# Optimization experiments

Hardware: AMD Instinct MI355X
Metric: run time of the kernel (lower is better)

Reference implementation:

```python
import jax, jax.numpy as jnp
import numpy as np

IN_DIM = 256
OUT_DIM = 256
B, N, E = 8, 1024, 262144
K_RATIO = 0.5
BN_EPS = 1e-5


def _xavier(key, shape):
    fan_in, fan_out = shape[1], shape[0]
    lim = float(np.sqrt(6.0 / (fan_in + fan_out)))
    return jax.random.uniform(key, shape, jnp.float32, -lim, lim)


def setup_inputs() -> dict:
    key = jax.random.key(0)
    ks = jax.random.split(key, 10)
    x = jax.random.normal(ks[0], (B, N, IN_DIM), jnp.float32)
    edges = jax.random.randint(ks[1], (2, E), 0, B * N, jnp.int64 if jax.config.jax_enable_x64 else jnp.int32)
    return {
        "x": x,
        "edges": edges,
        "att_proj_w": _xavier(ks[2], (OUT_DIM, IN_DIM)),
        "att_proj_b": jnp.zeros((OUT_DIM,), jnp.float32),
        "att_map_w": _xavier(ks[3], (1, OUT_DIM)).reshape(OUT_DIM),
        "pwa_w": _xavier(ks[4], (OUT_DIM, IN_DIM)),
        "pwa_b": jnp.zeros((OUT_DIM,), jnp.float32),
        "pwo_w": _xavier(ks[5], (OUT_DIM, IN_DIM)),
        "pwo_b": jnp.zeros((OUT_DIM,), jnp.float32),
        "bn_gamma": jnp.ones((OUT_DIM,), jnp.float32),
        "bn_beta": jnp.zeros((OUT_DIM,), jnp.float32),
        "y_w": _xavier(ks[6], (1, OUT_DIM)).reshape(OUT_DIM),
        "y_b": jnp.zeros((), jnp.float32),
    }


def reference(x, edges, att_proj_w, att_proj_b, att_map_w, pwa_w, pwa_b,
              pwo_w, pwo_b, bn_gamma, bn_beta, y_w, y_b):
    b, n, d = x.shape
    num_nodes = b * n
    xf = x.reshape(num_nodes, d)
    src, dst = edges[0], edges[1]  # x_j = source, x_i = destination

    # --- GAT message: alpha = att_map(tanh(att_proj(x_i * x_j))) ---
    x_j = xf[src]                                # [E, d]
    x_i = xf[dst]                                # [E, d]
    h = jnp.tanh((x_i * x_j) @ att_proj_w.T + att_proj_b)  # [E, out]
    alpha = h @ att_map_w                        # [E]

    # --- segment softmax over destination nodes ---
    amax = jax.ops.segment_max(alpha, dst, num_segments=num_nodes)
    a = jnp.exp(alpha - amax[dst])
    denom = jax.ops.segment_sum(a, dst, num_segments=num_nodes)
    w = a / (denom[dst] + 1e-16)

    # --- scatter-sum aggregate of alpha * x_j ---
    agg = jax.ops.segment_sum(w[:, None] * x_j, dst, num_segments=num_nodes)  # [num_nodes, d]

    out = agg @ pwa_w.T + pwa_b + xf @ pwo_w.T + pwo_b  # [num_nodes, out]

    # --- BatchNorm1d (training-mode batch stats, biased var) + SELU ---
    mean = out.mean(axis=0)
    var = out.var(axis=0)
    out = (out - mean) * jax.lax.rsqrt(var + BN_EPS) * bn_gamma + bn_beta
    out = jax.nn.selu(out)

    out = out.reshape(b, n, -1)  # [B, N, out]

    # --- GraphPool: top-k by sigmoid score, gate by score ---
    y = jax.nn.sigmoid(out @ y_w + y_b)  # [B, N]
    k = max(int(n * K_RATIO), 1)
    vals, ids = jax.lax.top_k(y, k)      # [B, k]
    x_top = jnp.take_along_axis(out, ids[..., None], axis=1)  # [B, k, out]
    return x_top * vals[..., None]
```

## Files before the change

kernel.cpp:

```cpp
#include <hip/hip_runtime.h>
#include <math.h>

#define NODES 8192
#define NEDGE 262144
#define DIM 256

typedef float f32x16 __attribute__((ext_vector_type(16)));
typedef _Float16 f16x8 __attribute__((ext_vector_type(8)));
typedef unsigned short u16;
typedef u16 u16x8 __attribute__((ext_vector_type(8)));
typedef u16 u16x4 __attribute__((ext_vector_type(4)));

__device__ __forceinline__ float fast_tanh(float x) {
    float t = __expf(2.f * x);
    return 1.f - 2.f * __builtin_amdgcn_rcpf(t + 1.f);
}

__device__ __forceinline__ u16 h_bits(_Float16 h) {
    u16 r; __builtin_memcpy(&r, &h, 2); return r;
}

__global__ void k_deg(const int* __restrict__ dst, int* __restrict__ deg) {
    int e = blockIdx.x * blockDim.x + threadIdx.x;
    if (e < NEDGE) atomicAdd(&deg[dst[e]], 1);
}

__global__ void k_scan(const int* __restrict__ deg, int* __restrict__ rowptr,
                       int* __restrict__ cursor) {
    __shared__ int part[256];
    int t = threadIdx.x;
    int base = t * 32;
    int local[32];
    int s = 0;
    for (int i = 0; i < 32; ++i) { local[i] = s; s += deg[base + i]; }
    part[t] = s;
    __syncthreads();
    for (int off = 1; off < 256; off <<= 1) {
        int v = (t >= off) ? part[t - off] : 0;
        __syncthreads();
        part[t] += v;
        __syncthreads();
    }
    int excl = (t == 0) ? 0 : part[t - 1];
    for (int i = 0; i < 32; ++i) {
        int v = excl + local[i];
        rowptr[base + i] = v;
        cursor[base + i] = v;
    }
    if (t == 255) rowptr[NODES] = part[255];
}

__global__ void k_fill(const int* __restrict__ src, const int* __restrict__ dst,
                       int* __restrict__ cursor, int2* __restrict__ sdg) {
    int e = blockIdx.x * blockDim.x + threadIdx.x;
    if (e < NEDGE) {
        int pos = atomicAdd(&cursor[dst[e]], 1);
        sdg[pos] = make_int2(src[e], dst[e]);
    }
}

__global__ void k_wfrag(const float* __restrict__ W, u16* __restrict__ wf) {
    int t = blockIdx.x * blockDim.x + threadIdx.x;
    if (t >= 16 * 4 * 2 * 64) return;
    int lane = t & 63;
    int mt = (t >> 6) & 1;
    int w = (t >> 7) & 3;
    int gks = t >> 9;
    int row = w * 64 + mt * 32 + (lane & 31);
    int k0 = gks * 16 + (lane >> 5) * 8;
    const float* p = W + (size_t)row * DIM + k0;
    u16x8 v1, v2;
#pragma unroll
    for (int j = 0; j < 8; ++j) {
        float f = p[j];
        _Float16 h1 = (_Float16)f;
        _Float16 h2 = (_Float16)((f - (float)h1) * 2048.f);
        v1[j] = h_bits(h1);
        v2[j] = h_bits(h2);
    }
    size_t base = ((size_t)(gks * 4 + w) * 4 + mt * 2) * 512 + lane * 8;
    *(u16x8*)(wf + base)       = v1;
    *(u16x8*)(wf + base + 512) = v2;
}

__global__ void k_wfrag2(const float* __restrict__ Wa, const float* __restrict__ Wo,
                         u16* __restrict__ wf2) {
    int t = blockIdx.x * blockDim.x + threadIdx.x;
    if (t >= 32 * 4 * 2 * 64) return;
    int lane = t & 63;
    int mt = (t >> 6) & 1;
    int w = (t >> 7) & 3;
    int gks = t >> 9;
    const float* W = (gks < 16) ? Wa : Wo;
    int row = w * 64 + mt * 32 + (lane & 31);
    int k0 = (gks & 15) * 16 + (lane >> 5) * 8;
    const float* p = W + (size_t)row * DIM + k0;
    u16x8 v1, v2;
#pragma unroll
    for (int j = 0; j < 8; ++j) {
        float f = p[j];
        _Float16 h1 = (_Float16)f;
        _Float16 h2 = (_Float16)((f - (float)h1) * 2048.f);
        v1[j] = h_bits(h1);
        v2[j] = h_bits(h2);
    }
    size_t base = ((size_t)(gks * 4 + w) * 4 + mt * 2) * 512 + lane * 8;
    *(u16x8*)(wf2 + base)       = v1;
    *(u16x8*)(wf2 + base + 512) = v2;
}

__global__ __launch_bounds__(256, 2) void k_alpha_v12(
    const float* __restrict__ x, const int2* __restrict__ sdg,
    const u16* __restrict__ wf, const float* __restrict__ bias,
    const float* __restrict__ amap, float* __restrict__ alpha_pos)
{
    __shared__ u16 p_lds[2][64][256];
    const int tid = threadIdx.x;
    const int w = tid >> 6;
    const int lane = tid & 63;
    const int l31 = lane & 31;
    const int g2 = lane >> 5;
    const int bid = blockIdx.x;
    const int wg = (bid & 7) * 512 + (bid >> 3);
    const int e0 = wg * 64;
    const int ebase = e0 + w * 16;
    const unsigned swz = ((unsigned)(l31 & 7)) << 4;

    f32x16 accM[2][2], accC[2][2];
#pragma unroll
    for (int mt = 0; mt < 2; ++mt)
#pragma unroll
        for (int nt = 0; nt < 2; ++nt) { accM[mt][nt] = (f32x16)0.f; accC[mt][nt] = (f32x16)0.f; }

    f16x8 afA[2][2], afB[2][2], afC[2][2];

#define PREFA(DST, GKS) { \
    const u16* pb_ = wf + ((size_t)((GKS) * 4 + w) * 4) * 512 + lane * 8; \
    _Pragma("unroll") for (int mt_ = 0; mt_ < 2; ++mt_) \
    _Pragma("unroll") for (int pl_ = 0; pl_ < 2; ++pl_) \
        DST[mt_][pl_] = *(const f16x8*)(const void*)(pb_ + (mt_ * 2 + pl_) * 512); }

#define KS(GKS, USE, PF) { \
    if ((GKS) + 2 < 16) { PREFA(PF, (GKS) + 2) } \
    f16x8 bfr[2][2]; \
    _Pragma("unroll") for (int nt_ = 0; nt_ < 2; ++nt_) { \
        const int en_ = nt_ * 32 + l31; \
        const unsigned off_ = ((unsigned)((GKS) * 32 + g2 * 16)) ^ swz; \
        _Pragma("unroll") for (int pl_ = 0; pl_ < 2; ++pl_) \
            bfr[nt_][pl_] = *(const f16x8*)(const void*)((const char*)&p_lds[pl_][en_][0] + off_); \
    } \
    _Pragma("unroll") for (int mt_ = 0; mt_ < 2; ++mt_) \
    _Pragma("unroll") for (int nt_ = 0; nt_ < 2; ++nt_) { \
        accM[mt_][nt_] = __builtin_amdgcn_mfma_f32_32x32x16_f16(USE[mt_][0], bfr[nt_][0], accM[mt_][nt_], 0, 0, 0); \
        accC[mt_][nt_] = __builtin_amdgcn_mfma_f32_32x32x16_f16(USE[mt_][0], bfr[nt_][1], accC[mt_][nt_], 0, 0, 0); \
        accC[mt_][nt_] = __builtin_amdgcn_mfma_f32_32x32x16_f16(USE[mt_][1], bfr[nt_][0], accC[mt_][nt_], 0, 0, 0); } }

    PREFA(afA, 0)
    PREFA(afB, 1)

#pragma unroll
    for (int i = 0; i < 16; ++i) {
        int2 sd = sdg[ebase + i];
        float4 a = *(const float4*)(x + (size_t)sd.x * DIM + lane * 4);
        float4 b = *(const float4*)(x + (size_t)sd.y * DIM + lane * 4);
        float pv[4] = {a.x * b.x, a.y * b.y, a.z * b.z, a.w * b.w};
        u16x4 v1, v2;
#pragma unroll
        for (int j = 0; j < 4; ++j) {
            float f = pv[j];
            _Float16 h1 = (_Float16)f;
            _Float16 h2 = (_Float16)((f - (float)h1) * 2048.f);
            v1[j] = h_bits(h1);
            v2[j] = h_bits(h2);
        }
        const int le = w * 16 + i;
        const unsigned off = ((unsigned)(lane * 8)) ^ (((unsigned)(le & 7)) << 4);
        *(u16x4*)((char*)&p_lds[0][le][0] + off) = v1;
        *(u16x4*)((char*)&p_lds[1][le][0] + off) = v2;
    }
    __syncthreads();

    KS(0,  afA, afC) KS(1,  afB, afA) KS(2,  afC, afB)
    KS(3,  afA, afC) KS(4,  afB, afA) KS(5,  afC, afB)
    KS(6,  afA, afC) KS(7,  afB, afA) KS(8,  afC, afB)
    KS(9,  afA, afC) KS(10, afB, afA) KS(11, afC, afB)
    KS(12, afA, afC) KS(13, afB, afA) KS(14, afC, afB)
    KS(15, afA, afC)
#undef KS
#undef PREFA

    float part[2] = {0.f, 0.f};
#pragma unroll
    for (int mt = 0; mt < 2; ++mt)
#pragma unroll
        for (int r = 0; r < 16; ++r) {
            int o = 64 * w + 32 * mt + (r & 3) + 8 * (r >> 2) + 4 * g2;
            float bo = bias[o], ao = amap[o];
#pragma unroll
            for (int nt = 0; nt < 2; ++nt) {
                float h = accM[mt][nt][r] + accC[mt][nt][r] * 4.8828125e-4f;
                part[nt] += ao * fast_tanh(h + bo);
            }
        }
    __syncthreads();
    float* red = (float*)(void*)p_lds;
#pragma unroll
    for (int nt = 0; nt < 2; ++nt) {
        float p = part[nt];
        p += __shfl_xor(p, 32);
        if (lane < 32) red[w * 64 + nt * 32 + lane] = p;
    }
    __syncthreads();
    if (tid < 64) alpha_pos[e0 + tid] = red[tid] + red[64 + tid] + red[128 + tid] + red[192 + tid];
}

__global__ void k_aggregate(
    const float* __restrict__ x, const float* __restrict__ alpha_pos,
    const int* __restrict__ rowptr, const int2* __restrict__ sdg,
    float* __restrict__ agg)
{
    int gw = (blockIdx.x * blockDim.x + threadIdx.x) >> 6;
    int lane = threadIdx.x & 63;
    if (gw >= NODES) return;
    int start = rowptr[gw], end = rowptr[gw + 1];
    int deg = end - start;
    float m = -INFINITY;
    for (int i = lane; i < deg; i += 64) m = fmaxf(m, alpha_pos[start + i]);
#pragma unroll
    for (int off = 32; off > 0; off >>= 1) m = fmaxf(m, __shfl_xor(m, off));
    float ssum = 0.f;
    for (int i = lane; i < deg; i += 64) ssum += expf(alpha_pos[start + i] - m);
#pragma unroll
    for (int off = 32; off > 0; off >>= 1) ssum += __shfl_xor(ssum, off);
    float a0 = 0.f, a1 = 0.f, a2 = 0.f, a3 = 0.f;
    int i = 0;
    for (; i + 4 <= deg; i += 4) {
        float w0 = expf(alpha_pos[start + i]     - m);
        float w1 = expf(alpha_pos[start + i + 1] - m);
        float w2 = expf(alpha_pos[start + i + 2] - m);
        float w3 = expf(alpha_pos[start + i + 3] - m);
        int r0 = sdg[start + i].x;
        int r1 = sdg[start + i + 1].x;
        int r2 = sdg[start + i + 2].x;
        int r3 = sdg[start + i + 3].x;
        float4 v0 = *(const float4*)(x + (size_t)r0 * DIM + lane * 4);
        float4 v1 = *(const float4*)(x + (size_t)r1 * DIM + lane * 4);
        float4 v2 = *(const float4*)(x + (size_t)r2 * DIM + lane * 4);
        float4 v3 = *(const float4*)(x + (size_t)r3 * DIM + lane * 4);
        a0 += w0 * v0.x + w1 * v1.x + w2 * v2.x + w3 * v3.x;
        a1 += w0 * v0.y + w1 * v1.y + w2 * v2.y + w3 * v3.y;
        a2 += w0 * v0.z + w1 * v1.z + w2 * v2.z + w3 * v3.z;
        a3 += w0 * v0.w + w1 * v1.w + w2 * v2.w + w3 * v3.w;
    }
    for (; i < deg; ++i) {
        float wgt = expf(alpha_pos[start + i] - m);
        int r = sdg[start + i].x;
        const float4 v = *(const float4*)(x + (size_t)r * DIM + lane * 4);
        a0 += wgt * v.x; a1 += wgt * v.y; a2 += wgt * v.z; a3 += wgt * v.w;
    }
    float inv = 1.f / (ssum + 1e-16f);
    float4 r; r.x = a0 * inv; r.y = a1 * inv; r.z = a2 * inv; r.w = a3 * inv;
    *(float4*)(agg + (size_t)gw * DIM + lane * 4) = r;
}

__global__ __launch_bounds__(256, 2) void k_out_mfma(
    const float* __restrict__ agg, const float* __restrict__ x,
    const u16* __restrict__ wf2, const float* __restrict__ ba,
    const float* __restrict__ bo, float* __restrict__ outb)
{
    __shared__ u16 p_lds[2][64][256];
    const int tid = threadIdx.x;
    const int w = tid >> 6;
    const int lane = tid & 63;
    const int l31 = lane & 31;
    const int g2 = lane >> 5;
    const int n0 = blockIdx.x * 64;
    const unsigned swz = ((unsigned)(l31 & 7)) << 4;

    f32x16 accM[2][2], accC[2][2];
#pragma unroll
    for (int mt = 0; mt < 2; ++mt)
#pragma unroll
        for (int nt = 0; nt < 2; ++nt) { accM[mt][nt] = (f32x16)0.f; accC[mt][nt] = (f32x16)0.f; }

    f16x8 afA[2][2], afB[2][2];

#define PREFA2(DST, GKS) { \
    const u16* pb_ = wf2 + ((size_t)((GKS) * 4 + w) * 4) * 512 + lane * 8; \
    _Pragma("unroll") for (int mt_ = 0; mt_ < 2; ++mt_) \
    _Pragma("unroll") for (int pl_ = 0; pl_ < 2; ++pl_) \
        DST[mt_][pl_] = *(const f16x8*)(const void*)(pb_ + (mt_ * 2 + pl_) * 512); }

#define OSTAGE(SRC) { \
    _Pragma("unroll") for (int i_ = 0; i_ < 16; ++i_) { \
        const int ln_ = w * 16 + i_; \
        float4 v_ = *(const float4*)((SRC) + (size_t)(n0 + ln_) * DIM + lane * 4); \
        float pv_[4] = {v_.x, v_.y, v_.z, v_.w}; \
        u16x4 v1_, v2_; \
        _Pragma("unroll") for (int j_ = 0; j_ < 4; ++j_) { \
            float f_ = pv_[j_]; \
            _Float16 h1_ = (_Float16)f_; \
            _Float16 h2_ = (_Float16)((f_ - (float)h1_) * 2048.f); \
            v1_[j_] = h_bits(h1_); v2_[j_] = h_bits(h2_); } \
        const unsigned off_ = ((unsigned)(lane * 8)) ^ (((unsigned)(ln_ & 7)) << 4); \
        *(u16x4*)((char*)&p_lds[0][ln_][0] + off_) = v1_; \
        *(u16x4*)((char*)&p_lds[1][ln_][0] + off_) = v2_; } }

#define OKSTEP(GKS) { \
    if ((GKS) + 1 < 32) { \
        if ((GKS) & 1) { PREFA2(afA, (GKS) + 1) } else { PREFA2(afB, (GKS) + 1) } \
    } \
    f16x8 bfr[2][2]; \
    _Pragma("unroll") for (int nt_ = 0; nt_ < 2; ++nt_) { \
        const int en_ = nt_ * 32 + l31; \
        const unsigned off_ = ((unsigned)(((GKS) & 15) * 32 + g2 * 16)) ^ swz; \
        _Pragma("unroll") for (int pl_ = 0; pl_ < 2; ++pl_) \
            bfr[nt_][pl_] = *(const f16x8*)(const void*)((const char*)&p_lds[pl_][en_][0] + off_); \
    } \
    _Pragma("unroll") for (int mt_ = 0; mt_ < 2; ++mt_) \
    _Pragma("unroll") for (int nt_ = 0; nt_ < 2; ++nt_) { \
        f16x8 a1_ = ((GKS) & 1) ? afB[mt_][0] : afA[mt_][0]; \
        f16x8 a2_ = ((GKS) & 1) ? afB[mt_][1] : afA[mt_][1]; \
        accM[mt_][nt_] = __builtin_amdgcn_mfma_f32_32x32x16_f16(a1_, bfr[nt_][0], accM[mt_][nt_], 0, 0, 0); \
        accC[mt_][nt_] = __builtin_amdgcn_mfma_f32_32x32x16_f16(a1_, bfr[nt_][1], accC[mt_][nt_], 0, 0, 0); \
        accC[mt_][nt_] = __builtin_amdgcn_mfma_f32_32x32x16_f16(a2_, bfr[nt_][0], accC[mt_][nt_], 0, 0, 0); } }

    PREFA2(afA, 0)
    OSTAGE(agg)
    __syncthreads();
    OKSTEP(0)  OKSTEP(1)  OKSTEP(2)  OKSTEP(3)
    OKSTEP(4)  OKSTEP(5)  OKSTEP(6)  OKSTEP(7)
    OKSTEP(8)  OKSTEP(9)  OKSTEP(10) OKSTEP(11)
    OKSTEP(12) OKSTEP(13) OKSTEP(14) OKSTEP(15)
    __syncthreads();
    OSTAGE(x)
    __syncthreads();
    OKSTEP(16) OKSTEP(17) OKSTEP(18) OKSTEP(19)
    OKSTEP(20) OKSTEP(21) OKSTEP(22) OKSTEP(23)
    OKSTEP(24) OKSTEP(25) OKSTEP(26) OKSTEP(27)
    OKSTEP(28) OKSTEP(29) OKSTEP(30) OKSTEP(31)
#undef OSTAGE
#undef OKSTEP
#undef PREFA2

    __syncthreads();
    float* Cs = (float*)(void*)p_lds;
#pragma unroll
    for (int mt = 0; mt < 2; ++mt)
#pragma unroll
        for (int r = 0; r < 16; ++r) {
            int o = 64 * w + 32 * mt + (r & 3) + 8 * (r >> 2) + 4 * g2;
            float bs = ba[o] + bo[o];
#pragma unroll
            for (int nt = 0; nt < 2; ++nt) {
                int col = nt * 32 + l31;
                float hv = accM[mt][nt][r] + accC[mt][nt][r] * 4.8828125e-4f + bs;
                unsigned ob = ((unsigned)(col * 1024 + o * 4)) ^ (((unsigned)(col & 31)) << 4);
                *(float*)((char*)Cs + ob) = hv;
            }
        }
    __syncthreads();
#pragma unroll
    for (int i = 0; i < 16; ++i) {
        int ln = w * 16 + i;
        unsigned rb = ((unsigned)(ln * 1024 + lane * 16)) ^ (((unsigned)(ln & 31)) << 4);
        float4 val = *(const float4*)((const char*)Cs + rb);
        *(float4*)(outb + (size_t)(n0 + ln) * DIM + lane * 4) = val;
    }
}

__global__ void k_colstat(const float* __restrict__ outb, double* __restrict__ psum,
                          double* __restrict__ psq) {
    int g = blockIdx.x, t = threadIdx.x;
    double s = 0.0, q = 0.0;
    const float* p = outb + (size_t)g * 256 * DIM + t;
    for (int r = 0; r < 256; ++r) { double v = (double)p[(size_t)r * DIM]; s += v; q += v * v; }
    psum[g * DIM + t] = s;
    psq[g * DIM + t] = q;
}

__global__ void k_bnparam(const double* __restrict__ psum, const double* __restrict__ psq,
                          const float* __restrict__ gamma, const float* __restrict__ beta,
                          float* __restrict__ scale, float* __restrict__ shift) {
    int t = threadIdx.x;
    double s = 0.0, q = 0.0;
    for (int g = 0; g < 32; ++g) { s += psum[g * DIM + t]; q += psq[g * DIM + t]; }
    double mean = s / (double)NODES;
    double var = q / (double)NODES - mean * mean;
    float sc = (float)((double)gamma[t] / sqrt(var + 1e-5));
    scale[t] = sc;
    shift[t] = (float)((double)beta[t] - mean * (double)sc);
}

__global__ void k_bnselu(float* __restrict__ outb, const float* __restrict__ scale,
                         const float* __restrict__ shift, const float* __restrict__ yw,
                         const float* __restrict__ yb, float* __restrict__ y) {
    int gw = (blockIdx.x * blockDim.x + threadIdx.x) >> 6;
    int lane = threadIdx.x & 63;
    if (gw >= NODES) return;
    float4 v  = *(const float4*)(outb + (size_t)gw * DIM + lane * 4);
    float4 sc = *(const float4*)(scale + lane * 4);
    float4 sh = *(const float4*)(shift + lane * 4);
    const float SL = 1.0507009873554805f, SA = 1.6732632423543772f;
    float4 o;
    o.x = v.x * sc.x + sh.x;
    o.y = v.y * sc.y + sh.y;
    o.z = v.z * sc.z + sh.z;
    o.w = v.w * sc.w + sh.w;
    o.x = (o.x > 0.f) ? SL * o.x : SL * SA * expm1f(o.x);
    o.y = (o.y > 0.f) ? SL * o.y : SL * SA * expm1f(o.y);
    o.z = (o.z > 0.f) ? SL * o.z : SL * SA * expm1f(o.z);
    o.w = (o.w > 0.f) ? SL * o.w : SL * SA * expm1f(o.w);
    *(float4*)(outb + (size_t)gw * DIM + lane * 4) = o;
    float4 w = *(const float4*)(yw + lane * 4);
    float z = o.x * w.x + o.y * w.y + o.z * w.z + o.w * w.w;
#pragma unroll
    for (int off = 32; off > 0; off >>= 1) z += __shfl_xor(z, off);
    if (lane == 0) y[gw] = 1.f / (1.f + expf(-(z + yb[0])));
}

__global__ void k_topk(const float* __restrict__ y, float* __restrict__ svals,
                       int* __restrict__ sidx) {
    __shared__ float v[1024];
    __shared__ int  id[1024];
    int b = blockIdx.x, t = threadIdx.x;
    v[t] = y[b * 1024 + t];           id[t] = t;
    v[t + 512] = y[b * 1024 + t + 512]; id[t + 512] = t + 512;
    __syncthreads();
    for (int k = 2; k <= 1024; k <<= 1) {
        for (int j = k >> 1; j > 0; j >>= 1) {
            for (int i = t; i < 1024; i += 512) {
                int l = i ^ j;
                if (l > i) {
                    float vi = v[i], vl = v[l];
                    int ii = id[i], il = id[l];
                    bool precede = (vi > vl) || (vi == vl && ii < il);
                    bool dirDesc = ((i & k) == 0);
                    bool sw = dirDesc ? !precede : precede;
                    if (sw) { v[i] = vl; v[l] = vi; id[i] = il; id[l] = ii; }
                }
            }
            __syncthreads();
        }
    }
    if (t < 512) { svals[b * 512 + t] = v[t]; sidx[b * 512 + t] = id[t]; }
}

__global__ void k_gather(const float* __restrict__ outb, const float* __restrict__ svals,
                         const int* __restrict__ sidx, float* __restrict__ dout) {
    int gw = (blockIdx.x * blockDim.x + threadIdx.x) >> 6;
    int lane = threadIdx.x & 63;
    int b = gw >> 9, r = gw & 511;
    float val = svals[b * 512 + r];
    int idn = sidx[b * 512 + r];
    float4 vv = *(const float4*)(outb + (size_t)(b * 1024 + idn) * DIM + lane * 4);
    vv.x *= val; vv.y *= val; vv.z *= val; vv.w *= val;
    *(float4*)(dout + (size_t)(b * 512 + r) * DIM + lane * 4) = vv;
}

extern "C" void kernel_launch(void* const* d_in, const int* in_sizes, int n_in,
                              void* d_out, int out_size, void* d_ws, size_t ws_size,
                              hipStream_t stream) {
    const float* x     = (const float*)d_in[0];
    const int* edges   = (const int*)d_in[1];
    const float* att_w = (const float*)d_in[2];
    const float* att_b = (const float*)d_in[3];
    const float* amap  = (const float*)d_in[4];
    const float* pwa_w = (const float*)d_in[5];
    const float* pwa_b = (const float*)d_in[6];
    const float* pwo_w = (const float*)d_in[7];
    const float* pwo_b = (const float*)d_in[8];
    const float* gamma = (const float*)d_in[9];
    const float* beta  = (const float*)d_in[10];
    const float* yw    = (const float*)d_in[11];
    const float* yb    = (const float*)d_in[12];
    float* out = (float*)d_out;
    const int* src = edges;
    const int* dst = edges + NEDGE;

    char* ws = (char*)d_ws;
    size_t off = 0;
    auto alloc = [&](size_t b) { void* p = ws + off; off = (off + b + 255) & ~(size_t)255; return p; };
    float* alpha  = (float*)alloc((size_t)NEDGE * 4);
    int2*  sdg    = (int2*)alloc((size_t)NEDGE * 8);
    float* agg    = (float*)alloc((size_t)NODES * DIM * 4);
    float* outb   = (float*)alloc((size_t)NODES * DIM * 4);
    int*   deg    = (int*)alloc(NODES * 4);
    int*   rowptr = (int*)alloc((NODES + 1) * 4);
    int*   cursor = (int*)alloc(NODES * 4);
    double* psum  = (double*)alloc(32 * DIM * 8);
    double* psq   = (double*)alloc(32 * DIM * 8);
    float* scale  = (float*)alloc(DIM * 4);
    float* shift  = (float*)alloc(DIM * 4);
    float* yv     = (float*)alloc(NODES * 4);
    float* svals  = (float*)alloc(8 * 512 * 4);
    int*   sidx   = (int*)alloc(8 * 512 * 4);
    u16*   wf     = (u16*)alloc((size_t)16 * 4 * 4 * 512 * 2);
    u16*   wf2    = (u16*)alloc((size_t)32 * 4 * 4 * 512 * 2);

    hipMemsetAsync(deg, 0, NODES * 4, stream);
    k_wfrag<<<32, 256, 0, stream>>>(att_w, wf);
    k_wfrag2<<<64, 256, 0, stream>>>(pwa_w, pwo_w, wf2);
    k_deg<<<NEDGE / 256, 256, 0, stream>>>(dst, deg);
    k_scan<<<1, 256, 0, stream>>>(deg, rowptr, cursor);
    k_fill<<<NEDGE / 256, 256, 0, stream>>>(src, dst, cursor, sdg);
    k_alpha_v12<<<NEDGE / 64, 256, 0, stream>>>(x, sdg, wf, att_b, amap, alpha);
    k_aggregate<<<NODES / 4, 256, 0, stream>>>(x, alpha, rowptr, sdg, agg);
    k_out_mfma<<<NODES / 64, 256, 0, stream>>>(agg, x, wf2, pwa_b, pwo_b, outb);
    k_colstat<<<32, 256, 0, stream>>>(outb, psum, psq);
    k_bnparam<<<1, 256, 0, stream>>>(psum, psq, gamma, beta, scale, shift);
    k_bnselu<<<NODES / 4, 256, 0, stream>>>(outb, scale, shift, yw, yb, yv);
    k_topk<<<8, 512, 0, stream>>>(yv, svals, sidx);
    k_gather<<<(8 * 512) / 4, 256, 0, stream>>>(outb, svals, sidx, out);
}
```

Measured before the change: 266.5 us.

## Warp-specialize alpha kernel into producer gather waves and MFMA consumer waves

Splits the alpha kernel's 512-thread block into four producer waves and four consumer waves. The producers gather x rows, form the elementwise products, split them into fp16 hi/lo parts and write them into double-buffered LDS half-tiles. The consumers run the MFMA tanh projection, so the gather of the next tile overlaps compute on the current one. Each block now handles 256 edges across four tiles, and each consumer wave writes its own partial alpha sum to global memory. A new small kernel adds the four partials, which costs extra global traffic and a launch, plus a block-wide barrier at every stage.

```diff
diff --git a/kernel.cpp b/kernel.cpp
--- a/kernel.cpp
+++ b/kernel.cpp
@@ -10,6 +10,7 @@
 typedef unsigned short u16;
 typedef u16 u16x8 __attribute__((ext_vector_type(8)));
 typedef u16 u16x4 __attribute__((ext_vector_type(4)));
+typedef u16 u16x2 __attribute__((ext_vector_type(2)));
 
 __device__ __forceinline__ float fast_tanh(float x) {
     float t = __expf(2.f * x);
@@ -109,30 +110,61 @@
     *(u16x8*)(wf2 + base + 512) = v2;
 }
 
-__global__ __launch_bounds__(256, 2) void k_alpha_v12(
+__global__ __launch_bounds__(512, 2) void k_alpha_v13(
     const float* __restrict__ x, const int2* __restrict__ sdg,
     const u16* __restrict__ wf, const float* __restrict__ bias,
-    const float* __restrict__ amap, float* __restrict__ alpha_pos)
+    const float* __restrict__ amap, float* __restrict__ apart)
 {
-    __shared__ u16 p_lds[2][64][256];
+    __shared__ u16 buf[2][2][64][128];
     const int tid = threadIdx.x;
-    const int w = tid >> 6;
+    const int wid = tid >> 6;
     const int lane = tid & 63;
-    const int l31 = lane & 31;
-    const int g2 = lane >> 5;
     const int bid = blockIdx.x;
-    const int wg = (bid & 7) * 512 + (bid >> 3);
-    const int e0 = wg * 64;
-    const int ebase = e0 + w * 16;
-    const unsigned swz = ((unsigned)(l31 & 7)) << 4;
-
-    f32x16 accM[2][2], accC[2][2];
-#pragma unroll
-    for (int mt = 0; mt < 2; ++mt)
-#pragma unroll
-        for (int nt = 0; nt < 2; ++nt) { accM[mt][nt] = (f32x16)0.f; accC[mt][nt] = (f32x16)0.f; }
-
-    f16x8 afA[2][2], afB[2][2], afC[2][2];
+    const int wg = (bid & 7) * 128 + (bid >> 3);
+    const int e0 = wg * 256;
+
+    if (wid >= 4) {
+        const int pw = wid - 4;
+#define STAGE(T, PH, B) { \
+    _Pragma("unroll") for (int i_ = 0; i_ < 16; ++i_) { \
+        const int le_ = pw * 16 + i_; \
+        int2 sd_ = sdg[e0 + (T) * 64 + le_]; \
+        float2 av_ = *(const float2*)(x + (size_t)sd_.x * DIM + (PH) * 128 + lane * 2); \
+        float2 bv_ = *(const float2*)(x + (size_t)sd_.y * DIM + (PH) * 128 + lane * 2); \
+        float p0_ = av_.x * bv_.x, p1_ = av_.y * bv_.y; \
+        _Float16 h10_ = (_Float16)p0_, h11_ = (_Float16)p1_; \
+        _Float16 h20_ = (_Float16)((p0_ - (float)h10_) * 2048.f); \
+        _Float16 h21_ = (_Float16)((p1_ - (float)h11_) * 2048.f); \
+        u16x2 v1_, v2_; \
+        v1_[0] = h_bits(h10_); v1_[1] = h_bits(h11_); \
+        v2_[0] = h_bits(h20_); v2_[1] = h_bits(h21_); \
+        const unsigned off_ = ((unsigned)(lane * 4)) ^ (((unsigned)(le_ & 7)) << 4); \
+        *(u16x2*)((char*)&buf[(B)][0][le_][0] + off_) = v1_; \
+        *(u16x2*)((char*)&buf[(B)][1][le_][0] + off_) = v2_; } }
+
+        STAGE(0, 0, 0) __syncthreads();
+        STAGE(0, 1, 1) __syncthreads();
+        STAGE(1, 0, 0) __syncthreads();
+        STAGE(1, 1, 1) __syncthreads();
+        STAGE(2, 0, 0) __syncthreads();
+        STAGE(2, 1, 1) __syncthreads();
+        STAGE(3, 0, 0) __syncthreads();
+        STAGE(3, 1, 1) __syncthreads();
+        __syncthreads();
+#undef STAGE
+    } else {
+        const int w = wid;
+        const int l31 = lane & 31;
+        const int g2 = lane >> 5;
+        const unsigned swz = ((unsigned)(l31 & 7)) << 4;
+
+        f32x16 accM[2][2], accC[2][2];
+#pragma unroll
+        for (int mt = 0; mt < 2; ++mt)
+#pragma unroll
+            for (int nt = 0; nt < 2; ++nt) { accM[mt][nt] = (f32x16)0.f; accC[mt][nt] = (f32x16)0.f; }
+
+        f16x8 afA[2][2], afB[2][2], afC[2][2];
 
 #define PREFA(DST, GKS) { \
     const u16* pb_ = wf + ((size_t)((GKS) * 4 + w) * 4) * 512 + lane * 8; \
@@ -140,14 +172,14 @@
     _Pragma("unroll") for (int pl_ = 0; pl_ < 2; ++pl_) \
         DST[mt_][pl_] = *(const f16x8*)(const void*)(pb_ + (mt_ * 2 + pl_) * 512); }
 
-#define KS(GKS, USE, PF) { \
-    if ((GKS) + 2 < 16) { PREFA(PF, (GKS) + 2) } \
+#define KS(LKS, GA, B, USE, PF) { \
+    PREFA(PF, ((GA) + 2) & 15) \
     f16x8 bfr[2][2]; \
     _Pragma("unroll") for (int nt_ = 0; nt_ < 2; ++nt_) { \
         const int en_ = nt_ * 32 + l31; \
-        const unsigned off_ = ((unsigned)((GKS) * 32 + g2 * 16)) ^ swz; \
+        const unsigned off_ = ((unsigned)((LKS) * 32 + g2 * 16)) ^ swz; \
         _Pragma("unroll") for (int pl_ = 0; pl_ < 2; ++pl_) \
-            bfr[nt_][pl_] = *(const f16x8*)(const void*)((const char*)&p_lds[pl_][en_][0] + off_); \
+            bfr[nt_][pl_] = *(const f16x8*)(const void*)((const char*)&buf[(B)][pl_][en_][0] + off_); \
     } \
     _Pragma("unroll") for (int mt_ = 0; mt_ < 2; ++mt_) \
     _Pragma("unroll") for (int nt_ = 0; nt_ < 2; ++nt_) { \
@@ -155,63 +187,51 @@
         accC[mt_][nt_] = __builtin_amdgcn_mfma_f32_32x32x16_f16(USE[mt_][0], bfr[nt_][1], accC[mt_][nt_], 0, 0, 0); \
         accC[mt_][nt_] = __builtin_amdgcn_mfma_f32_32x32x16_f16(USE[mt_][1], bfr[nt_][0], accC[mt_][nt_], 0, 0, 0); } }
 
-    PREFA(afA, 0)
-    PREFA(afB, 1)
-
-#pragma unroll
-    for (int i = 0; i < 16; ++i) {
-        int2 sd = sdg[ebase + i];
-        float4 a = *(const float4*)(x + (size_t)sd.x * DIM + lane * 4);
-        float4 b = *(const float4*)(x + (size_t)sd.y * DIM + lane * 4);
-        float pv[4] = {a.x * b.x, a.y * b.y, a.z * b.z, a.w * b.w};
-        u16x4 v1, v2;
-#pragma unroll
-        for (int j = 0; j < 4; ++j) {
-            float f = pv[j];
-            _Float16 h1 = (_Float16)f;
-            _Float16 h2 = (_Float16)((f - (float)h1) * 2048.f);
-            v1[j] = h_bits(h1);
-            v2[j] = h_bits(h2);
-        }
-        const int le = w * 16 + i;
-        const unsigned off = ((unsigned)(lane * 8)) ^ (((unsigned)(le & 7)) << 4);
-        *(u16x4*)((char*)&p_lds[0][le][0] + off) = v1;
-        *(u16x4*)((char*)&p_lds[1][le][0] + off) = v2;
-    }
-    __syncthreads();
-
-    KS(0,  afA, afC) KS(1,  afB, afA) KS(2,  afC, afB)
-    KS(3,  afA, afC) KS(4,  afB, afA) KS(5,  afC, afB)
-    KS(6,  afA, afC) KS(7,  afB, afA) KS(8,  afC, afB)
-    KS(9,  afA, afC) KS(10, afB, afA) KS(11, afC, afB)
-    KS(12, afA, afC) KS(13, afB, afA) KS(14, afC, afB)
-    KS(15, afA, afC)
+#define PH8(B, G, X, Y, Z) \
+    KS(0,(G)+0,B,X,Z) KS(1,(G)+1,B,Y,X) KS(2,(G)+2,B,Z,Y) KS(3,(G)+3,B,X,Z) \
+    KS(4,(G)+4,B,Y,X) KS(5,(G)+5,B,Z,Y) KS(6,(G)+6,B,X,Z) KS(7,(G)+7,B,Y,X)
+
+#define EPI(T) { \
+    float part0 = 0.f, part1 = 0.f; \
+    _Pragma("unroll") for (int mt_ = 0; mt_ < 2; ++mt_) \
+    _Pragma("unroll") for (int r_ = 0; r_ < 16; ++r_) { \
+        int o_ = 64 * w + 32 * mt_ + (r_ & 3) + 8 * (r_ >> 2) + 4 * g2; \
+        float bo_ = bias[o_], ao_ = amap[o_]; \
+        float h0_ = accM[mt_][0][r_] + accC[mt_][0][r_] * 4.8828125e-4f; \
+        float h1_ = accM[mt_][1][r_] + accC[mt_][1][r_] * 4.8828125e-4f; \
+        part0 += ao_ * fast_tanh(h0_ + bo_); \
+        part1 += ao_ * fast_tanh(h1_ + bo_); \
+    } \
+    part0 += __shfl_xor(part0, 32); \
+    part1 += __shfl_xor(part1, 32); \
+    if (lane < 32) { \
+        apart[(size_t)w * NEDGE + e0 + (T) * 64 + lane] = part0; \
+        apart[(size_t)w * NEDGE + e0 + (T) * 64 + 32 + lane] = part1; \
+    } \
+    _Pragma("unroll") for (int mt_ = 0; mt_ < 2; ++mt_) \
+    _Pragma("unroll") for (int nt_ = 0; nt_ < 2; ++nt_) { accM[mt_][nt_] = (f32x16)0.f; accC[mt_][nt_] = (f32x16)0.f; } }
+
+        PREFA(afA, 0)
+        PREFA(afB, 1)
+        __syncthreads();
+        PH8(0, 0, afA, afB, afC) __syncthreads();
+        PH8(1, 8, afC, afA, afB) EPI(0) __syncthreads();
+        PH8(0, 0, afB, afC, afA) __syncthreads();
+        PH8(1, 8, afA, afB, afC) EPI(1) __syncthreads();
+        PH8(0, 0, afC, afA, afB) __syncthreads();
+        PH8(1, 8, afB, afC, afA) EPI(2) __syncthreads();
+        PH8(0, 0, afA, afB, afC) __syncthreads();
+        PH8(1, 8, afC, afA, afB) EPI(3) __syncthreads();
+#undef PREFA
 #undef KS
-#undef PREFA
-
-    float part[2] = {0.f, 0.f};
-#pragma unroll
-    for (int mt = 0; mt < 2; ++mt)
-#pragma unroll
-        for (int r = 0; r < 16; ++r) {
-            int o = 64 * w + 32 * mt + (r & 3) + 8 * (r >> 2) + 4 * g2;
-            float bo = bias[o], ao = amap[o];
-#pragma unroll
-            for (int nt = 0; nt < 2; ++nt) {
-                float h = accM[mt][nt][r] + accC[mt][nt][r] * 4.8828125e-4f;
-                part[nt] += ao * fast_tanh(h + bo);
-            }
-        }
-    __syncthreads();
-    float* red = (float*)(void*)p_lds;
-#pragma unroll
-    for (int nt = 0; nt < 2; ++nt) {
-        float p = part[nt];
-        p += __shfl_xor(p, 32);
-        if (lane < 32) red[w * 64 + nt * 32 + lane] = p;
-    }
-    __syncthreads();
-    if (tid < 64) alpha_pos[e0 + tid] = red[tid] + red[64 + tid] + red[128 + tid] + red[192 + tid];
+#undef PH8
+#undef EPI
+    }
+}
+
+__global__ void k_asum(const float* __restrict__ apart, float* __restrict__ alpha) {
+    int i = blockIdx.x * blockDim.x + threadIdx.x;
+    alpha[i] = ((apart[i] + apart[NEDGE + i]) + apart[2 * NEDGE + i]) + apart[3 * NEDGE + i];
 }
 
 __global__ void k_aggregate(
@@ -482,6 +502,7 @@
     size_t off = 0;
     auto alloc = [&](size_t b) { void* p = ws + off; off = (off + b + 255) & ~(size_t)255; return p; };
     float* alpha  = (float*)alloc((size_t)NEDGE * 4);
+    float* apart  = (float*)alloc((size_t)4 * NEDGE * 4);
     int2*  sdg    = (int2*)alloc((size_t)NEDGE * 8);
     float* agg    = (float*)alloc((size_t)NODES * DIM * 4);
     float* outb   = (float*)alloc((size_t)NODES * DIM * 4);
@@ -504,7 +525,8 @@
     k_deg<<<NEDGE / 256, 256, 0, stream>>>(dst, deg);
     k_scan<<<1, 256, 0, stream>>>(deg, rowptr, cursor);
     k_fill<<<NEDGE / 256, 256, 0, stream>>>(src, dst, cursor, sdg);
-    k_alpha_v12<<<NEDGE / 64, 256, 0, stream>>>(x, sdg, wf, att_b, amap, alpha);
+    k_alpha_v13<<<NEDGE / 256, 512, 0, stream>>>(x, sdg, wf, att_b, amap, apart);
+    k_asum<<<NEDGE / 256, 256, 0, stream>>>(apart, alpha);
     k_aggregate<<<NODES / 4, 256, 0, stream>>>(x, alpha, rowptr, sdg, agg);
     k_out_mfma<<<NODES / 64, 256, 0, stream>>>(agg, x, wf2, pwa_b, pwo_b, outb);
     k_colstat<<<32, 256, 0, stream>>>(outb, psum, psq);
```

After: 294.8 us. 1.11x slower.

## Fuse BN column statistics into output GEMM epilogue and merge weight-prep kernels

Applied to the files above, without the earlier changes.

Column sum and sum-of-squares for BatchNorm are now computed in the epilogue of the output MFMA kernel, reduced across waves in LDS and written as per-block float partials. This removes the separate k_colstat pass that re-read the whole output buffer. The two weight-fragment prep kernels are merged into one launch, and the fp16 hi/lo split uses packed round-toward-zero conversions. The trade-offs are float instead of double partial accumulation, and RTZ instead of round-to-nearest in the split, which may slightly change precision.

```diff
diff --git a/kernel.cpp b/kernel.cpp
--- a/kernel.cpp
+++ b/kernel.cpp
@@ -7,6 +7,7 @@
 
 typedef float f32x16 __attribute__((ext_vector_type(16)));
 typedef _Float16 f16x8 __attribute__((ext_vector_type(8)));
+typedef __fp16 h16x2 __attribute__((ext_vector_type(2)));
 typedef unsigned short u16;
 typedef u16 u16x8 __attribute__((ext_vector_type(8)));
 typedef u16 u16x4 __attribute__((ext_vector_type(4)));
@@ -18,6 +19,22 @@
 
 __device__ __forceinline__ u16 h_bits(_Float16 h) {
     u16 r; __builtin_memcpy(&r, &h, 2); return r;
+}
+
+union SplitU { h16x2 h2[2]; u16x4 u4; };
+
+__device__ __forceinline__ void split4(float p0, float p1, float p2, float p3,
+                                       u16x4& v1, u16x4& v2) {
+    h16x2 h01 = __builtin_amdgcn_cvt_pkrtz(p0, p1);
+    h16x2 h23 = __builtin_amdgcn_cvt_pkrtz(p2, p3);
+    h16x2 r01 = __builtin_amdgcn_cvt_pkrtz((p0 - (float)h01[0]) * 2048.f,
+                                           (p1 - (float)h01[1]) * 2048.f);
+    h16x2 r23 = __builtin_amdgcn_cvt_pkrtz((p2 - (float)h23[0]) * 2048.f,
+                                           (p3 - (float)h23[1]) * 2048.f);
+    SplitU c1, c2;
+    c1.h2[0] = h01; c1.h2[1] = h23;
+    c2.h2[0] = r01; c2.h2[1] = r23;
+    v1 = c1.u4; v2 = c2.u4;
 }
 
 __global__ void k_deg(const int* __restrict__ dst, int* __restrict__ deg) {
@@ -59,16 +76,25 @@
     }
 }
 
-__global__ void k_wfrag(const float* __restrict__ W, u16* __restrict__ wf) {
+__global__ void k_wfrag_all(const float* __restrict__ W, const float* __restrict__ Wa,
+                            const float* __restrict__ Wo, u16* __restrict__ wf,
+                            u16* __restrict__ wf2) {
     int t = blockIdx.x * blockDim.x + threadIdx.x;
-    if (t >= 16 * 4 * 2 * 64) return;
-    int lane = t & 63;
-    int mt = (t >> 6) & 1;
-    int w = (t >> 7) & 3;
-    int gks = t >> 9;
+    const float* S;
+    u16* D;
+    int gks, w, mt, lane;
+    if (t < 8192) {
+        lane = t & 63; mt = (t >> 6) & 1; w = (t >> 7) & 3; gks = t >> 9;
+        S = W; D = wf;
+    } else {
+        int t2 = t - 8192;
+        if (t2 >= 16384) return;
+        lane = t2 & 63; mt = (t2 >> 6) & 1; w = (t2 >> 7) & 3; gks = t2 >> 9;
+        S = (gks < 16) ? Wa : Wo; D = wf2;
+    }
     int row = w * 64 + mt * 32 + (lane & 31);
-    int k0 = gks * 16 + (lane >> 5) * 8;
-    const float* p = W + (size_t)row * DIM + k0;
+    int k0 = (gks & 15) * 16 + (lane >> 5) * 8;
+    const float* p = S + (size_t)row * DIM + k0;
     u16x8 v1, v2;
 #pragma unroll
     for (int j = 0; j < 8; ++j) {
@@ -79,37 +105,11 @@
         v2[j] = h_bits(h2);
     }
     size_t base = ((size_t)(gks * 4 + w) * 4 + mt * 2) * 512 + lane * 8;
-    *(u16x8*)(wf + base)       = v1;
-    *(u16x8*)(wf + base + 512) = v2;
-}
-
-__global__ void k_wfrag2(const float* __restrict__ Wa, const float* __restrict__ Wo,
-                         u16* __restrict__ wf2) {
-    int t = blockIdx.x * blockDim.x + threadIdx.x;
-    if (t >= 32 * 4 * 2 * 64) return;
-    int lane = t & 63;
-    int mt = (t >> 6) & 1;
-    int w = (t >> 7) & 3;
-    int gks = t >> 9;
-    const float* W = (gks < 16) ? Wa : Wo;
-    int row = w * 64 + mt * 32 + (lane & 31);
-    int k0 = (gks & 15) * 16 + (lane >> 5) * 8;
-    const float* p = W + (size_t)row * DIM + k0;
-    u16x8 v1, v2;
-#pragma unroll
-    for (int j = 0; j < 8; ++j) {
-        float f = p[j];
-        _Float16 h1 = (_Float16)f;
-        _Float16 h2 = (_Float16)((f - (float)h1) * 2048.f);
-        v1[j] = h_bits(h1);
-        v2[j] = h_bits(h2);
-    }
-    size_t base = ((size_t)(gks * 4 + w) * 4 + mt * 2) * 512 + lane * 8;
-    *(u16x8*)(wf2 + base)       = v1;
-    *(u16x8*)(wf2 + base + 512) = v2;
-}
-
-__global__ __launch_bounds__(256, 2) void k_alpha_v12(
+    *(u16x8*)(D + base)       = v1;
+    *(u16x8*)(D + base + 512) = v2;
+}
+
+__global__ __launch_bounds__(256, 2) void k_alpha_v15(
     const float* __restrict__ x, const int2* __restrict__ sdg,
     const u16* __restrict__ wf, const float* __restrict__ bias,
     const float* __restrict__ amap, float* __restrict__ alpha_pos)
@@ -163,16 +163,8 @@
         int2 sd = sdg[ebase + i];
         float4 a = *(const float4*)(x + (size_t)sd.x * DIM + lane * 4);
         float4 b = *(const float4*)(x + (size_t)sd.y * DIM + lane * 4);
-        float pv[4] = {a.x * b.x, a.y * b.y, a.z * b.z, a.w * b.w};
         u16x4 v1, v2;
-#pragma unroll
-        for (int j = 0; j < 4; ++j) {
-            float f = pv[j];
-            _Float16 h1 = (_Float16)f;
-            _Float16 h2 = (_Float16)((f - (float)h1) * 2048.f);
-            v1[j] = h_bits(h1);
-            v2[j] = h_bits(h2);
-        }
+        split4(a.x * b.x, a.y * b.y, a.z * b.z, a.w * b.w, v1, v2);
         const int le = w * 16 + i;
         const unsigned off = ((unsigned)(lane * 8)) ^ (((unsigned)(le & 7)) << 4);
         *(u16x4*)((char*)&p_lds[0][le][0] + off) = v1;
@@ -266,7 +258,8 @@
 __global__ __launch_bounds__(256, 2) void k_out_mfma(
     const float* __restrict__ agg, const float* __restrict__ x,
     const u16* __restrict__ wf2, const float* __restrict__ ba,
-    const float* __restrict__ bo, float* __restrict__ outb)
+    const float* __restrict__ bo, float* __restrict__ outb,
+    float* __restrict__ psumf, float* __restrict__ psqf)
 {
     __shared__ u16 p_lds[2][64][256];
     const int tid = threadIdx.x;
@@ -295,13 +288,8 @@
     _Pragma("unroll") for (int i_ = 0; i_ < 16; ++i_) { \
         const int ln_ = w * 16 + i_; \
         float4 v_ = *(const float4*)((SRC) + (size_t)(n0 + ln_) * DIM + lane * 4); \
-        float pv_[4] = {v_.x, v_.y, v_.z, v_.w}; \
         u16x4 v1_, v2_; \
-        _Pragma("unroll") for (int j_ = 0; j_ < 4; ++j_) { \
-            float f_ = pv_[j_]; \
-            _Float16 h1_ = (_Float16)f_; \
-            _Float16 h2_ = (_Float16)((f_ - (float)h1_) * 2048.f); \
-            v1_[j_] = h_bits(h1_); v2_[j_] = h_bits(h2_); } \
+        split4(v_.x, v_.y, v_.z, v_.w, v1_, v2_); \
         const unsigned off_ = ((unsigned)(lane * 8)) ^ (((unsigned)(ln_ & 7)) << 4); \
         *(u16x4*)((char*)&p_lds[0][ln_][0] + off_) = v1_; \
         *(u16x4*)((char*)&p_lds[1][ln_][0] + off_) = v2_; } }
@@ -360,31 +348,41 @@
             }
         }
     __syncthreads();
+    float s4[4] = {0.f, 0.f, 0.f, 0.f};
+    float q4[4] = {0.f, 0.f, 0.f, 0.f};
 #pragma unroll
     for (int i = 0; i < 16; ++i) {
         int ln = w * 16 + i;
         unsigned rb = ((unsigned)(ln * 1024 + lane * 16)) ^ (((unsigned)(ln & 31)) << 4);
         float4 val = *(const float4*)((const char*)Cs + rb);
         *(float4*)(outb + (size_t)(n0 + ln) * DIM + lane * 4) = val;
-    }
-}
-
-__global__ void k_colstat(const float* __restrict__ outb, double* __restrict__ psum,
-                          double* __restrict__ psq) {
-    int g = blockIdx.x, t = threadIdx.x;
-    double s = 0.0, q = 0.0;
-    const float* p = outb + (size_t)g * 256 * DIM + t;
-    for (int r = 0; r < 256; ++r) { double v = (double)p[(size_t)r * DIM]; s += v; q += v * v; }
-    psum[g * DIM + t] = s;
-    psq[g * DIM + t] = q;
-}
-
-__global__ void k_bnparam(const double* __restrict__ psum, const double* __restrict__ psq,
+        s4[0] += val.x; s4[1] += val.y; s4[2] += val.z; s4[3] += val.w;
+        q4[0] += val.x * val.x; q4[1] += val.y * val.y;
+        q4[2] += val.z * val.z; q4[3] += val.w * val.w;
+    }
+    __syncthreads();
+    float* rs = (float*)(void*)p_lds;
+#pragma unroll
+    for (int j = 0; j < 4; ++j) {
+        rs[w * 256 + lane * 4 + j] = s4[j];
+        rs[1024 + w * 256 + lane * 4 + j] = q4[j];
+    }
+    __syncthreads();
+    if (tid < 256) {
+        int c = tid;
+        float ssum = rs[c] + rs[256 + c] + rs[512 + c] + rs[768 + c];
+        float qsum = rs[1024 + c] + rs[1280 + c] + rs[1536 + c] + rs[1792 + c];
+        psumf[blockIdx.x * 256 + c] = ssum;
+        psqf[blockIdx.x * 256 + c] = qsum;
+    }
+}
+
+__global__ void k_bnparam(const float* __restrict__ psumf, const float* __restrict__ psqf,
                           const float* __restrict__ gamma, const float* __restrict__ beta,
                           float* __restrict__ scale, float* __restrict__ shift) {
     int t = threadIdx.x;
     double s = 0.0, q = 0.0;
-    for (int g = 0; g < 32; ++g) { s += psum[g * DIM + t]; q += psq[g * DIM + t]; }
+    for (int g = 0; g < 128; ++g) { s += (double)psumf[g * DIM + t]; q += (double)psqf[g * DIM + t]; }
     double mean = s / (double)NODES;
     double var = q / (double)NODES - mean * mean;
     float sc = (float)((double)gamma[t] / sqrt(var + 1e-5));
@@ -488,8 +486,8 @@
     int*   deg    = (int*)alloc(NODES * 4);
     int*   rowptr = (int*)alloc((NODES + 1) * 4);
     int*   cursor = (int*)alloc(NODES * 4);
-    double* psum  = (double*)alloc(32 * DIM * 8);
-    double* psq   = (double*)alloc(32 * DIM * 8);
+    float* psumf  = (float*)alloc(128 * DIM * 4);
+    float* psqf   = (float*)alloc(128 * DIM * 4);
     float* scale  = (float*)alloc(DIM * 4);
     float* shift  = (float*)alloc(DIM * 4);
     float* yv     = (float*)alloc(NODES * 4);
@@ -498,17 +496,15 @@
     u16*   wf     = (u16*)alloc((size_t)16 * 4 * 4 * 512 * 2);
     u16*   wf2    = (u16*)alloc((size_t)32 * 4 * 4 * 512 * 2);
 
-    hipMemsetAsync(deg, 0, NODES * 4, stream);
-    k_wfrag<<<32, 256, 0, stream>>>(att_w, wf);
-    k_wfrag2<<<64, 256, 0, stream>>>(pwa_w, pwo_w, wf2);
+    (void)hipMemsetAsync(deg, 0, NODES * 4, stream);
+    k_wfrag_all<<<96, 256, 0, stream>>>(att_w, pwa_w, pwo_w, wf, wf2);
     k_deg<<<NEDGE / 256, 256, 0, stream>>>(dst, deg);
     k_scan<<<1, 256, 0, stream>>>(deg, rowptr, cursor);
     k_fill<<<NEDGE / 256, 256, 0, stream>>>(src, dst, cursor, sdg);
-    k_alpha_v12<<<NEDGE / 64, 256, 0, stream>>>(x, sdg, wf, att_b, amap, alpha);
+    k_alpha_v15<<<NEDGE / 64, 256, 0, stream>>>(x, sdg, wf, att_b, amap, alpha);
     k_aggregate<<<NODES / 4, 256, 0, stream>>>(x, alpha, rowptr, sdg, agg);
-    k_out_mfma<<<NODES / 64, 256, 0, stream>>>(agg, x, wf2, pwa_b, pwo_b, outb);
-    k_colstat<<<32, 256, 0, stream>>>(outb, psum, psq);
-    k_bnparam<<<1, 256, 0, stream>>>(psum, psq, gamma, beta, scale, shift);
+    k_out_mfma<<<NODES / 64, 256, 0, stream>>>(agg, x, wf2, pwa_b, pwo_b, outb, psumf, psqf);
+    k_bnparam<<<1, 256, 0, stream>>>(psumf, psqf, gamma, beta, scale, shift);
     k_bnselu<<<NODES / 4, 256, 0, stream>>>(outb, scale, shift, yw, yb, yv);
     k_topk<<<8, 512, 0, stream>>>(yv, svals, sidx);
     k_gather<<<(8 * 512) / 4, 256, 0, stream>>>(outb, svals, sidx, out);
```

Result: faster. 258.1 us (-3.1%).
